# Performance work log

Measured on AMD Instinct MI355X. Metric: run time of the kernel, lower is better.

## Reference

```python
import jax, jax.numpy as jnp
import numpy as np

HEADS = 4
DIM_HEAD = 32
LN_EPS = 1e-5


def _ln_linear(x, g, b, W, bias):
    # LayerNorm over last dim then Linear (W stored as [in, out])
    mu = x.mean(-1, keepdims=True)
    var = ((x - mu) ** 2).mean(-1, keepdims=True)
    xn = (x - mu) * jax.lax.rsqrt(var + LN_EPS) * g + b
    return xn @ W + bias


def setup_inputs() -> dict:
    key = jax.random.key(0)
    ks = jax.random.split(key, 12)
    b, n, X, Y, W1, W2, d = 1, 6, 8, 8, 8, 8, 128
    x, y, w1, w2 = 8, 8, 8, 10
    inner = HEADS * DIM_HEAD  # 128
    s = 1.0 / np.sqrt(d)
    inp = {
        'q': jax.random.normal(ks[0], (b, n, X, Y, W1, W2, d), jnp.float32),
        'k': jax.random.normal(ks[1], (b, n, x, y, w1, w2, d), jnp.float32),
        'v': jax.random.normal(ks[2], (b, n, x, y, w1, w2, d), jnp.float32),
        'skip': jax.random.normal(ks[3], (b, X, Y, W1, W2, d), jnp.float32),
        'attn_scale': jnp.full((b,), 1.2, jnp.float32),
        'lnq_g': jnp.ones((d,), jnp.float32), 'lnq_b': jnp.zeros((d,), jnp.float32),
        'Wq': jax.random.normal(ks[4], (d, inner), jnp.float32) * s,
        'bq': jnp.zeros((inner,), jnp.float32),
        'lnk_g': jnp.ones((d,), jnp.float32), 'lnk_b': jnp.zeros((d,), jnp.float32),
        'Wk': jax.random.normal(ks[5], (d, inner), jnp.float32) * s,
        'bk': jnp.zeros((inner,), jnp.float32),
        'lnv_g': jnp.ones((d,), jnp.float32), 'lnv_b': jnp.zeros((d,), jnp.float32),
        'Wv': jax.random.normal(ks[6], (d, inner), jnp.float32) * s,
        'bv': jnp.zeros((inner,), jnp.float32),
        'Wp': jax.random.normal(ks[7], (inner, d), jnp.float32) * s,
        'bp': jnp.zeros((d,), jnp.float32),
    }
    return inp


def reference(q, k, v, skip, attn_scale, lnq_g, lnq_b, Wq, bq, lnk_g, lnk_b, Wk, bk,
              lnv_g, lnv_b, Wv, bv, Wp, bp):
    b, n, X, Y, W1, W2, d = q.shape
    _, _, x, y, w1, w2, _ = k.shape
    m, dh = HEADS, DIM_HEAD
    scale = dh ** -0.5
    # 'b n x y w1 w2 d -> b (x y) (n w1 w2) d'
    qf = jnp.transpose(q, (0, 2, 3, 1, 4, 5, 6)).reshape(b, X * Y, n * W1 * W2, d)
    kf = jnp.transpose(k, (0, 2, 3, 1, 4, 5, 6)).reshape(b, x * y, n * w1 * w2, d)
    vf = jnp.transpose(v, (0, 2, 3, 1, 4, 5, 6)).reshape(b, x * y, n * w1 * w2, d)
    qp = _ln_linear(qf, lnq_g, lnq_b, Wq, bq)
    kp = _ln_linear(kf, lnk_g, lnk_b, Wk, bk)
    vp = _ln_linear(vf, lnv_g, lnv_b, Wv, bv)

    def split_heads(t):  # 'b L N (m d) -> (b m) L N d'
        B, L, N, _ = t.shape
        return jnp.transpose(t.reshape(B, L, N, m, dh), (0, 3, 1, 2, 4)).reshape(B * m, L, N, dh)

    qh, kh, vh = split_heads(qp), split_heads(kp), split_heads(vp)
    dot = scale * jnp.einsum('blqd,blkd->blqk', qh, kh)  # (b*m, L, Q, K)
    # per-batch scale factor repeated over heads (b-major, matching einops '(b m)')
    sv = jnp.repeat(attn_scale.reshape(-1), m)
    dot = dot * sv[:, None, None, None]
    att = jax.nn.softmax(dot, axis=-1)
    a = jnp.einsum('blqk,blkd->blqd', att, vh)
    # '(b m) L N d -> b L N (m d)'
    a = jnp.transpose(a.reshape(b, m, X * Y, n * W1 * W2, dh), (0, 2, 3, 1, 4))
    a = a.reshape(b, X * Y, n * W1 * W2, m * dh)
    # 'b (x y) (n w1 w2) d -> b n x y w1 w2 d'
    a = a.reshape(b, X, Y, n, W1, W2, m * dh)
    a = jnp.transpose(a, (0, 3, 1, 2, 4, 5, 6))
    z = a @ Wp + bp        # proj
    z = z.mean(axis=1)     # mean over views n
    return z + skip
```

## Files before the change

kernel.cpp:

```cpp
#include <hip/hip_runtime.h>

#define D 128
#define LN_EPS 1e-5f
#define WSTR 136

typedef __attribute__((ext_vector_type(8))) short short8;
typedef __attribute__((ext_vector_type(4))) float f32x4;

static __device__ __forceinline__ unsigned short f2bf(float f) {
    union { float f; unsigned u; } v; v.f = f;
    unsigned r = v.u + 0x7fffu + ((v.u >> 16) & 1u);
    return (unsigned short)(r >> 16);
}
static __device__ __forceinline__ unsigned pack2(float a, float b) {
    return (unsigned)f2bf(a) | ((unsigned)f2bf(b) << 16);
}
static __device__ __forceinline__ float bf2f(unsigned short u) {
    union { unsigned u; float f; } v; v.u = ((unsigned)u) << 16; return v.f;
}

__global__ __launch_bounds__(64)
void wprep_kernel(const float* __restrict__ Wq, const float* __restrict__ Wk,
                  const float* __restrict__ Wv, const float* __restrict__ Wp,
                  const float* __restrict__ gq, const float* __restrict__ betaq,
                  const float* __restrict__ biasq,
                  const float* __restrict__ gk, const float* __restrict__ betak,
                  const float* __restrict__ biask,
                  const float* __restrict__ gv, const float* __restrict__ betav,
                  const float* __restrict__ biasv,
                  unsigned* __restrict__ Wt, unsigned* __restrict__ Wpt,
                  float* __restrict__ c1, float* __restrict__ c2)
{
    const int id = blockIdx.x;
    const int w  = id >> 7;
    const int o  = id & 127;
    const int t  = threadIdx.x;
    if (w < 3) {
        const float* W  = (w == 0) ? Wq : (w == 1) ? Wk : Wv;
        const float* gg = (w == 0) ? gq : (w == 1) ? gk : gv;
        const float* bb = (w == 0) ? betaq : (w == 1) ? betak : betav;
        const float* bi = (w == 0) ? biasq : (w == 1) ? biask : biasv;
        const float w0 = W[(2 * t) * 128 + o];
        const float w1 = W[(2 * t + 1) * 128 + o];
        const float g0 = gg[2 * t], g1 = gg[2 * t + 1];
        const float b0 = bb[2 * t], b1 = bb[2 * t + 1];
        Wt[((size_t)w * 128 + o) * 64 + t] = pack2(g0 * w0, g1 * w1);
        float s1 = g0 * w0 + g1 * w1;
        float s2 = b0 * w0 + b1 * w1;
        #pragma unroll
        for (int off = 32; off > 0; off >>= 1) {
            s1 += __shfl_down(s1, off, 64);
            s2 += __shfl_down(s2, off, 64);
        }
        if (t == 0) { c1[w * 128 + o] = s1; c2[w * 128 + o] = s2 + bi[o]; }
    } else {
        Wpt[(size_t)o * 64 + t] = pack2(Wp[(2 * t) * 128 + o], Wp[(2 * t + 1) * 128 + o]);
    }
}

template<int PERL, int W1W2, int W2D, int MODE>
static __device__ __forceinline__
void ln_body(const float* __restrict__ in,
             const unsigned short* __restrict__ wlds,
             const float* __restrict__ c1, const float* __restrict__ c2,
             unsigned short* __restrict__ out,
             float scale, int rowbase, int t,
             float (*smu)[16], float (*ssq)[16])
{
    const int wv   = t >> 6;
    const int lane = t & 63;
    const int m16  = lane & 15;
    const int g    = lane >> 4;
    const int row  = rowbase + wv * 16 + m16;

    const int l   = row / PERL, j = row - l * PERL;
    const int n   = j / W1W2, rem = j - n * W1W2;
    const int w1  = rem / W2D, w2 = rem - w1 * W2D;
    const int X   = l >> 3, Y = l & 7;
    const float* xrow = in + ((size_t)(((n * 8 + X) * 8 + Y) * 8 + w1) * W2D + w2) * D;

    short8 xf[4];
    #pragma unroll
    for (int kt = 0; kt < 4; ++kt) {
        const float4 a = *(const float4*)(xrow + kt * 32 + g * 8);
        const float4 b = *(const float4*)(xrow + kt * 32 + g * 8 + 4);
        short8 vv;
        vv[0] = (short)f2bf(a.x); vv[1] = (short)f2bf(a.y);
        vv[2] = (short)f2bf(a.z); vv[3] = (short)f2bf(a.w);
        vv[4] = (short)f2bf(b.x); vv[5] = (short)f2bf(b.y);
        vv[6] = (short)f2bf(b.z); vv[7] = (short)f2bf(b.w);
        xf[kt] = vv;
    }

    short8 ones;
    #pragma unroll
    for (int jj = 0; jj < 8; ++jj) ones[jj] = (short)0x3F80;
    f32x4 sums = {0.f, 0.f, 0.f, 0.f}, gram = {0.f, 0.f, 0.f, 0.f};
    #pragma unroll
    for (int kt = 0; kt < 4; ++kt) {
        sums = __builtin_amdgcn_mfma_f32_16x16x32_bf16(xf[kt], ones, sums, 0, 0, 0);
        gram = __builtin_amdgcn_mfma_f32_16x16x32_bf16(xf[kt], xf[kt], gram, 0, 0, 0);
    }
    if (g == (m16 >> 2)) {
        smu[wv][m16] = sums[m16 & 3];
        ssq[wv][m16] = gram[m16 & 3];
    }
    __syncthreads();
    const float mu   = smu[wv][m16] * (1.0f / 128.0f);
    const float msq  = ssq[wv][m16] * (1.0f / 128.0f);
    const float rstd = rsqrtf(msq - mu * mu + LN_EPS);
    const float rmu  = rstd * mu;

    f32x4 acc[8] = {{0,0,0,0},{0,0,0,0},{0,0,0,0},{0,0,0,0},
                    {0,0,0,0},{0,0,0,0},{0,0,0,0},{0,0,0,0}};
    #pragma unroll
    for (int kt = 0; kt < 4; ++kt) {
        #pragma unroll
        for (int ot = 0; ot < 8; ++ot) {
            const short8 aw = *(const short8*)&wlds[
                (ot * 16 + m16) * WSTR + kt * 32 + g * 8];
            acc[ot] = __builtin_amdgcn_mfma_f32_16x16x32_bf16(aw, xf[kt], acc[ot], 0, 0, 0);
        }
    }

    #pragma unroll
    for (int ot = 0; ot < 8; ++ot) {
        const int ob = ot * 16 + g * 4;
        const float4 cc1 = *(const float4*)&c1[ob];
        const float4 cc2 = *(const float4*)&c2[ob];
        float v0 = rstd * acc[ot][0] - rmu * cc1.x + cc2.x;
        float v1 = rstd * acc[ot][1] - rmu * cc1.y + cc2.y;
        float v2 = rstd * acc[ot][2] - rmu * cc1.z + cc2.z;
        float v3 = rstd * acc[ot][3] - rmu * cc1.w + cc2.w;
        if (MODE == 1) { v0 *= scale; v1 *= scale; v2 *= scale; v3 *= scale; }
        if (MODE == 2) {
            const float vals[4] = {v0, v1, v2, v3};
            #pragma unroll
            for (int c = 0; c < 4; ++c) {
                const int d = ob + c;
                out[((size_t)((l * 4 + (d >> 5)) * 32 + (d & 31))) * 480 + j] = f2bf(vals[c]);
            }
        } else {
            *(ushort4*)&out[(size_t)row * D + ob] =
                make_ushort4(f2bf(v0), f2bf(v1), f2bf(v2), f2bf(v3));
        }
    }
}

__global__ __launch_bounds__(256, 4)
void ln_fused_kernel(const float* __restrict__ q, const float* __restrict__ k,
                     const float* __restrict__ v,
                     const unsigned short* __restrict__ Wt,
                     const float* __restrict__ c1, const float* __restrict__ c2,
                     unsigned short* __restrict__ qbuf,
                     unsigned short* __restrict__ kbuf,
                     unsigned short* __restrict__ vtb,
                     const float* __restrict__ scale_p)
{
    __shared__ __align__(16) unsigned short wlds[128 * WSTR];
    __shared__ float smu[4][16];
    __shared__ float ssq[4][16];

    const int bid = blockIdx.x;
    const int t   = threadIdx.x;

    const unsigned short* Wsrc =
        (bid < 384) ? Wt : (bid < 864) ? (Wt + 16384) : (Wt + 32768);

    {
        const uint4* ws = (const uint4*)Wsrc;
        #pragma unroll
        for (int i = 0; i < 8; ++i) {
            const int idx = i * 256 + t;
            const int r = idx >> 4, s = idx & 15;
            *(uint4*)&wlds[r * WSTR + s * 8] = ws[idx];
        }
    }
    __syncthreads();

    if (bid < 384) {
        const float s = scale_p[0] * 0.17677669529663687f * 1.4426950408889634f;
        ln_body<384, 64, 8, 1>(q, wlds, c1, c2, qbuf, s, bid * 64, t, smu, ssq);
    } else if (bid < 864) {
        ln_body<480, 80, 10, 0>(k, wlds, c1 + 128, c2 + 128, kbuf,
                                1.0f, (bid - 384) * 64, t, smu, ssq);
    } else {
        ln_body<480, 80, 10, 2>(v, wlds, c1 + 256, c2 + 256, vtb,
                                1.0f, (bid - 864) * 64, t, smu, ssq);
    }
}

__global__ __launch_bounds__(256, 4)
void attn_kernel(const unsigned short* __restrict__ qb,
                 const unsigned short* __restrict__ kb,
                 const unsigned short* __restrict__ vtb,
                 unsigned short* __restrict__ out)
{
    const int l    = blockIdx.x;
    const int h    = blockIdx.y;
    const int qz   = blockIdx.z;
    const int t    = threadIdx.x;
    const int wv   = t >> 6;
    const int lane = t & 63;
    const int m16  = lane & 15;
    const int g    = lane >> 4;

    short8 bq[3];
    #pragma unroll
    for (int qt = 0; qt < 3; ++qt) {
        const int qrow0 = qz * 192 + qt * 64 + wv * 16;
        bq[qt] = *(const short8*)(
            qb + ((size_t)(l * 384 + qrow0 + m16)) * 128 + h * 32 + g * 8);
    }

    const unsigned short* kbase = kb + ((size_t)l * 480) * 128 + h * 32;
    const unsigned short* vbase = vtb + ((size_t)(l * 4 + h) * 32) * 480;

    f32x4 o0[3] = {{0,0,0,0},{0,0,0,0},{0,0,0,0}};
    f32x4 o1[3] = {{0,0,0,0},{0,0,0,0},{0,0,0,0}};
    float esum[3] = {0.f, 0.f, 0.f};

    const int srcA = m16 + (g & 1) * 32;
    const int srcB = srcA + 16;
    const bool lo  = (g < 2);

    short8 a0n = *(const short8*)(kbase + (size_t)(m16) * 128 + g * 8);
    short8 a1n = *(const short8*)(kbase + (size_t)(16 + m16) * 128 + g * 8);
    short8 v0n = *(const short8*)(vbase + (size_t)m16 * 480 + g * 8);
    short8 v1n = *(const short8*)(vbase + (size_t)(16 + m16) * 480 + g * 8);

    for (int kc = 0; kc < 15; ++kc) {
        const short8 a0 = a0n, a1 = a1n, v0 = v0n, v1 = v1n;
        if (kc < 14) {
            const int kn = (kc + 1) * 32;
            a0n = *(const short8*)(kbase + (size_t)(kn + m16) * 128 + g * 8);
            a1n = *(const short8*)(kbase + (size_t)(kn + 16 + m16) * 128 + g * 8);
            v0n = *(const short8*)(vbase + (size_t)m16 * 480 + kn + g * 8);
            v1n = *(const short8*)(vbase + (size_t)(16 + m16) * 480 + kn + g * 8);
        }

        #pragma unroll
        for (int qt = 0; qt < 3; ++qt) {
            const f32x4 z = {0.f, 0.f, 0.f, 0.f};
            const f32x4 s0 = __builtin_amdgcn_mfma_f32_16x16x32_bf16(a0, bq[qt], z, 0, 0, 0);
            const f32x4 s1 = __builtin_amdgcn_mfma_f32_16x16x32_bf16(a1, bq[qt], z, 0, 0, 0);

            float e0[4], e1[4];
            float es = 0.f;
            #pragma unroll
            for (int r = 0; r < 4; ++r) {
                e0[r] = __builtin_amdgcn_exp2f(s0[r]);
                e1[r] = __builtin_amdgcn_exp2f(s1[r]);
                es += e0[r] + e1[r];
            }
            esum[qt] += es;

            const unsigned pA0 = pack2(e0[0], e0[1]);
            const unsigned pA1 = pack2(e0[2], e0[3]);
            const unsigned pB0 = pack2(e1[0], e1[1]);
            const unsigned pB1 = pack2(e1[2], e1[3]);

            const unsigned uA0 = __shfl(pA0, srcA, 64);
            const unsigned uA1 = __shfl(pA1, srcA, 64);
            const unsigned uA2 = __shfl(pA0, srcB, 64);
            const unsigned uA3 = __shfl(pA1, srcB, 64);
            const unsigned uB0 = __shfl(pB0, srcA, 64);
            const unsigned uB1 = __shfl(pB1, srcA, 64);
            const unsigned uB2 = __shfl(pB0, srcB, 64);
            const unsigned uB3 = __shfl(pB1, srcB, 64);

            union { unsigned u[4]; short8 s; } bp;
            bp.u[0] = lo ? uA0 : uB0;
            bp.u[1] = lo ? uA1 : uB1;
            bp.u[2] = lo ? uA2 : uB2;
            bp.u[3] = lo ? uA3 : uB3;

            o0[qt] = __builtin_amdgcn_mfma_f32_16x16x32_bf16(v0, bp.s, o0[qt], 0, 0, 0);
            o1[qt] = __builtin_amdgcn_mfma_f32_16x16x32_bf16(v1, bp.s, o1[qt], 0, 0, 0);
        }
    }

    #pragma unroll
    for (int qt = 0; qt < 3; ++qt) {
        float lsum = esum[qt];
        lsum += __shfl_xor(lsum, 16, 64);
        lsum += __shfl_xor(lsum, 32, 64);
        const float linv = 1.0f / lsum;

        const int qrow0 = qz * 192 + qt * 64 + wv * 16;
        unsigned short* ob = out + ((size_t)(l * 384 + qrow0 + m16)) * 128 + h * 32;
        *(ushort4*)(ob + g * 4) = make_ushort4(
            f2bf(o0[qt][0] * linv), f2bf(o0[qt][1] * linv),
            f2bf(o0[qt][2] * linv), f2bf(o0[qt][3] * linv));
        *(ushort4*)(ob + 16 + g * 4) = make_ushort4(
            f2bf(o1[qt][0] * linv), f2bf(o1[qt][1] * linv),
            f2bf(o1[qt][2] * linv), f2bf(o1[qt][3] * linv));
    }
}

__global__ __launch_bounds__(256)
void proj_kernel(const unsigned short* __restrict__ attnb,
                 const unsigned short* __restrict__ Wpt,
                 const float* __restrict__ bp,
                 const float* __restrict__ skip,
                 float* __restrict__ out)
{
    const int t    = threadIdx.x;
    const int wv   = t >> 6;
    const int lane = t & 63;
    const int m16  = lane & 15;
    const int g    = lane >> 4;

    const int row  = blockIdx.x * 16 + m16;
    const int l    = row >> 6;
    const int qrem = row & 63;

    short8 xf[4];
    #pragma unroll
    for (int kt = 0; kt < 4; ++kt) {
        float m[8] = {0,0,0,0,0,0,0,0};
        #pragma unroll
        for (int n = 0; n < 6; ++n) {
            const short8 vv = *(const short8*)(
                attnb + ((size_t)(l * 384 + n * 64 + qrem)) * 128 + kt * 32 + g * 8);
            #pragma unroll
            for (int jj = 0; jj < 8; ++jj)
                m[jj] += bf2f((unsigned short)vv[jj]);
        }
        short8 pk;
        #pragma unroll
        for (int jj = 0; jj < 8; ++jj) pk[jj] = (short)f2bf(m[jj] * (1.0f / 6.0f));
        xf[kt] = pk;
    }

    f32x4 acc[2] = {{0,0,0,0},{0,0,0,0}};
    #pragma unroll
    for (int kt = 0; kt < 4; ++kt) {
        #pragma unroll
        for (int ot = 0; ot < 2; ++ot) {
            const short8 aw = *(const short8*)&Wpt[
                (size_t)((wv * 2 + ot) * 16 + m16) * 128 + kt * 32 + g * 8];
            acc[ot] = __builtin_amdgcn_mfma_f32_16x16x32_bf16(aw, xf[kt], acc[ot], 0, 0, 0);
        }
    }

    #pragma unroll
    for (int ot = 0; ot < 2; ++ot) {
        const int ob = (wv * 2 + ot) * 16 + g * 4;
        const float4 bb = *(const float4*)&bp[ob];
        const float4 sk = *(const float4*)&skip[(size_t)row * D + ob];
        float4 r;
        r.x = acc[ot][0] + bb.x + sk.x;
        r.y = acc[ot][1] + bb.y + sk.y;
        r.z = acc[ot][2] + bb.z + sk.z;
        r.w = acc[ot][3] + bb.w + sk.w;
        *(float4*)&out[(size_t)row * D + ob] = r;
    }
}

extern "C" void kernel_launch(void* const* d_in, const int* in_sizes, int n_in,
                              void* d_out, int out_size, void* d_ws, size_t ws_size,
                              hipStream_t stream)
{
    const float* q          = (const float*)d_in[0];
    const float* k          = (const float*)d_in[1];
    const float* v          = (const float*)d_in[2];
    const float* skip       = (const float*)d_in[3];
    const float* attn_scale = (const float*)d_in[4];
    const float* lnq_g      = (const float*)d_in[5];
    const float* lnq_b      = (const float*)d_in[6];
    const float* Wq         = (const float*)d_in[7];
    const float* bq         = (const float*)d_in[8];
    const float* lnk_g      = (const float*)d_in[9];
    const float* lnk_b      = (const float*)d_in[10];
    const float* Wk         = (const float*)d_in[11];
    const float* bk         = (const float*)d_in[12];
    const float* lnv_g      = (const float*)d_in[13];
    const float* lnv_b      = (const float*)d_in[14];
    const float* Wv         = (const float*)d_in[15];
    const float* bv         = (const float*)d_in[16];
    const float* Wp         = (const float*)d_in[17];
    const float* bp         = (const float*)d_in[18];

    float* out = (float*)d_out;
    char*  wsb = (char*)d_ws;

    unsigned short* qbuf  = (unsigned short*)(wsb);
    unsigned short* kbuf  = (unsigned short*)(wsb + 6291456);
    unsigned short* vtb   = (unsigned short*)(wsb + 14155776);
    unsigned short* Wt    = (unsigned short*)(wsb + 22020096);
    unsigned short* Wpt   = (unsigned short*)(wsb + 22118400);
    float*          c1    = (float*)        (wsb + 22151168);
    float*          c2    = (float*)        (wsb + 22152704);
    unsigned short* attnb = (unsigned short*)(wsb + 22154240);

    wprep_kernel<<<512, 64, 0, stream>>>(Wq, Wk, Wv, Wp,
                                         lnq_g, lnq_b, bq,
                                         lnk_g, lnk_b, bk,
                                         lnv_g, lnv_b, bv,
                                         (unsigned*)Wt, (unsigned*)Wpt, c1, c2);

    ln_fused_kernel<<<1344, 256, 0, stream>>>(q, k, v, Wt, c1, c2,
                                              qbuf, kbuf, vtb, attn_scale);

    dim3 agrid(64, 4, 2);
    attn_kernel<<<agrid, 256, 0, stream>>>(qbuf, kbuf, vtb, attnb);

    proj_kernel<<<256, 256, 0, stream>>>(attnb, Wpt, bp, skip, out);
}
```

Before: 150.7 us.

## Fold mean over views into attention epilogue, write per-half partial sums

Each attention block now sums its three query tiles (which correspond to three views for the same spatial position) in registers and writes one partial sum per half of the view range, instead of writing every view's output. The projection kernel then reads two partial rows instead of six and averages them. This cuts the intermediate attention buffer traffic by a factor of three on both write and read. It adds an extra bf16 rounding on the partial sums before the final mean.

```diff
diff --git a/kernel.cpp b/kernel.cpp
--- a/kernel.cpp
+++ b/kernel.cpp
@@ -194,7 +194,7 @@
 void attn_kernel(const unsigned short* __restrict__ qb,
                  const unsigned short* __restrict__ kb,
                  const unsigned short* __restrict__ vtb,
-                 unsigned short* __restrict__ out)
+                 unsigned short* __restrict__ pmean)
 {
     const int l    = blockIdx.x;
     const int h    = blockIdx.y;
@@ -280,26 +280,31 @@
         }
     }
 
+    f32x4 om0 = {0.f, 0.f, 0.f, 0.f};
+    f32x4 om1 = {0.f, 0.f, 0.f, 0.f};
     #pragma unroll
     for (int qt = 0; qt < 3; ++qt) {
         float lsum = esum[qt];
         lsum += __shfl_xor(lsum, 16, 64);
         lsum += __shfl_xor(lsum, 32, 64);
         const float linv = 1.0f / lsum;
-
-        const int qrow0 = qz * 192 + qt * 64 + wv * 16;
-        unsigned short* ob = out + ((size_t)(l * 384 + qrow0 + m16)) * 128 + h * 32;
-        *(ushort4*)(ob + g * 4) = make_ushort4(
-            f2bf(o0[qt][0] * linv), f2bf(o0[qt][1] * linv),
-            f2bf(o0[qt][2] * linv), f2bf(o0[qt][3] * linv));
-        *(ushort4*)(ob + 16 + g * 4) = make_ushort4(
-            f2bf(o1[qt][0] * linv), f2bf(o1[qt][1] * linv),
-            f2bf(o1[qt][2] * linv), f2bf(o1[qt][3] * linv));
-    }
+        #pragma unroll
+        for (int r = 0; r < 4; ++r) {
+            om0[r] += o0[qt][r] * linv;
+            om1[r] += o1[qt][r] * linv;
+        }
+    }
+
+    const int pos = wv * 16 + m16;
+    unsigned short* ob = pmean + ((size_t)qz * 4096 + l * 64 + pos) * 128 + h * 32;
+    *(ushort4*)(ob + g * 4) = make_ushort4(
+        f2bf(om0[0]), f2bf(om0[1]), f2bf(om0[2]), f2bf(om0[3]));
+    *(ushort4*)(ob + 16 + g * 4) = make_ushort4(
+        f2bf(om1[0]), f2bf(om1[1]), f2bf(om1[2]), f2bf(om1[3]));
 }
 
 __global__ __launch_bounds__(256)
-void proj_kernel(const unsigned short* __restrict__ attnb,
+void proj_kernel(const unsigned short* __restrict__ pmean,
                  const unsigned short* __restrict__ Wpt,
                  const float* __restrict__ bp,
                  const float* __restrict__ skip,
@@ -312,24 +317,21 @@
     const int g    = lane >> 4;
 
     const int row  = blockIdx.x * 16 + m16;
-    const int l    = row >> 6;
-    const int qrem = row & 63;
 
     short8 xf[4];
     #pragma unroll
     for (int kt = 0; kt < 4; ++kt) {
-        float m[8] = {0,0,0,0,0,0,0,0};
-        #pragma unroll
-        for (int n = 0; n < 6; ++n) {
-            const short8 vv = *(const short8*)(
-                attnb + ((size_t)(l * 384 + n * 64 + qrem)) * 128 + kt * 32 + g * 8);
-            #pragma unroll
-            for (int jj = 0; jj < 8; ++jj)
-                m[jj] += bf2f((unsigned short)vv[jj]);
-        }
+        const short8 p0 = *(const short8*)(
+            pmean + (size_t)row * 128 + kt * 32 + g * 8);
+        const short8 p1 = *(const short8*)(
+            pmean + (size_t)4096 * 128 + (size_t)row * 128 + kt * 32 + g * 8);
         short8 pk;
         #pragma unroll
-        for (int jj = 0; jj < 8; ++jj) pk[jj] = (short)f2bf(m[jj] * (1.0f / 6.0f));
+        for (int jj = 0; jj < 8; ++jj) {
+            const float m = (bf2f((unsigned short)p0[jj]) +
+                             bf2f((unsigned short)p1[jj])) * (1.0f / 6.0f);
+            pk[jj] = (short)f2bf(m);
+        }
         xf[kt] = pk;
     }
 
@@ -392,7 +394,7 @@
     unsigned short* Wpt   = (unsigned short*)(wsb + 22118400);
     float*          c1    = (float*)        (wsb + 22151168);
     float*          c2    = (float*)        (wsb + 22152704);
-    unsigned short* attnb = (unsigned short*)(wsb + 22154240);
+    unsigned short* pmean = (unsigned short*)(wsb + 22154240);
 
     wprep_kernel<<<512, 64, 0, stream>>>(Wq, Wk, Wv, Wp,
                                          lnq_g, lnq_b, bq,
@@ -404,7 +406,7 @@
                                               qbuf, kbuf, vtb, attn_scale);
 
     dim3 agrid(64, 4, 2);
-    attn_kernel<<<agrid, 256, 0, stream>>>(qbuf, kbuf, vtb, attnb);
-
-    proj_kernel<<<256, 256, 0, stream>>>(attnb, Wpt, bp, skip, out);
-}
+    attn_kernel<<<agrid, 256, 0, stream>>>(qbuf, kbuf, vtb, pmean);
+
+    proj_kernel<<<256, 256, 0, stream>>>(pmean, Wpt, bp, skip, out);
+}
```

Result: no change. 147.8 us, median of 2 (-1.9%).
